# Performance work log

Measured on AMD Instinct MI355X. Metric: run time of the kernel, lower is better.

The kernel has to match this reference:

```python
import jax, jax.numpy as jnp
import numpy as np

# Dimensions
B_, T_, IN_ = 8, 1024, 512          # batch, seq_len, in_dim
D_ = 1024                           # latent_dim (hidden_size)
I_ = 2048                           # intermediate_size
N_ = 64                             # state_size
H_ = 16                             # ssm_num_head
P_ = I_ // H_                       # head_dim = 128
K_ = 3                              # conv_kernel
L_ = 4                              # num_layer
OUT_, CB_ = 512, 1024               # out_dim, num_code_book
CONV_DIM = I_ + 2 * N_              # 2176
PROJ = I_ + CONV_DIM + H_           # in_proj width of mixer = 4240


def setup_inputs() -> dict:
    key = jax.random.key(0)
    ks = jax.random.split(key, 16)
    s = 0.02
    inp = {
        "x": jax.random.normal(ks[0], (B_, T_, IN_), jnp.float32),
        "in_w": jax.random.normal(ks[1], (IN_, D_), jnp.float32) * s,
        "in_b": jnp.zeros((D_,), jnp.float32),
        "norm_w": jnp.ones((L_, D_), jnp.float32),
        "mix_in_w": jax.random.normal(ks[2], (L_, D_, PROJ), jnp.float32) * s,
        "conv_w": jax.random.normal(ks[3], (L_, K_, 1, CONV_DIM), jnp.float32) * s,
        "conv_b": jnp.zeros((L_, CONV_DIM), jnp.float32),
        "dt_bias": jax.random.normal(ks[4], (L_, H_), jnp.float32) * 0.1,
        "A_log": jnp.log(jax.random.uniform(ks[5], (L_, H_), jnp.float32, 0.001, 0.1)),
        "D": jnp.ones((L_, H_), jnp.float32),
        "gnorm_w": jnp.ones((L_, I_), jnp.float32),
        "mix_out_w": jax.random.normal(ks[6], (L_, I_, D_), jnp.float32) * s,
        "out_w": jax.random.normal(ks[7], (D_, OUT_), jnp.float32) * s,
        "out_b": jnp.zeros((OUT_,), jnp.float32),
        "code_w": jax.random.normal(ks[8], (D_, CB_), jnp.float32) * s,
        "code_b": jnp.zeros((CB_,), jnp.float32),
    }
    return inp


def rmsnorm(x, w, eps=1e-6):
    v = jnp.mean(jnp.square(x), axis=-1, keepdims=True)
    return x * jax.lax.rsqrt(v + eps) * w


def mamba_block(x, nw, inw, cw, cb, dtb, alog, Dv, gnw, outw):
    residual = x
    h = rmsnorm(x, nw)
    proj = h @ inw                                   # [B,T,PROJ]
    gate, hBC, dt = jnp.split(proj, [I_, I_ + CONV_DIM], axis=-1)
    # causal depthwise conv along time
    conv = jax.lax.conv_general_dilated(
        hBC, cw, window_strides=(1,), padding=[(K_ - 1, 0)],
        dimension_numbers=("NWC", "WIO", "NWC"), feature_group_count=CONV_DIM)
    conv = jax.nn.silu(conv + cb)
    xs, Bm, Cm = jnp.split(conv, [I_, I_ + N_], axis=-1)   # [B,T,I],[B,T,N],[B,T,N]
    dt = jax.nn.softplus(dt + dtb)                   # [B,T,H]
    a = -jnp.exp(alog)                               # [H] scalar decay per head
    xh = xs.reshape(B_, T_, H_, P_)

    def step(hst, inp):
        dt_t, B_t, C_t, x_t = inp                    # [B,H],[B,N],[B,N],[B,H,P]
        dA = jnp.exp(dt_t * a)                       # [B,H]
        hst = hst * dA[:, :, None, None] + (dt_t[:, :, None, None] * x_t[..., None]) * B_t[:, None, None, :]
        y = jnp.einsum("bhpn,bn->bhp", hst, C_t)
        return hst, y

    inputs = (dt.transpose(1, 0, 2), Bm.transpose(1, 0, 2),
              Cm.transpose(1, 0, 2), xh.transpose(1, 0, 2, 3))
    h0 = jnp.zeros((B_, H_, P_, N_), x.dtype)
    _, ys = jax.lax.scan(step, h0, inputs)           # ys: [T,B,H,P]
    y = ys.transpose(1, 0, 2, 3) + Dv[None, None, :, None] * xh
    y = y.reshape(B_, T_, I_)
    y = rmsnorm(y * jax.nn.silu(gate), gnw)          # gated RMSNorm
    return residual + y @ outw


def reference(x, in_w, in_b, norm_w, mix_in_w, conv_w, conv_b, dt_bias,
              A_log, D, gnorm_w, mix_out_w, out_w, out_b, code_w, code_b):
    h = x @ in_w + in_b
    for i in range(L_):
        h = mamba_block(h, norm_w[i], mix_in_w[i], conv_w[i], conv_b[i],
                        dt_bias[i], A_log[i], D[i], gnorm_w[i], mix_out_w[i])
    return (h @ out_w + out_b, h @ code_w + code_b)
```

## Files before the change

kernel.cpp:

```cpp
#include <hip/hip_runtime.h>
#include <hip/hip_bf16.h>

typedef __hip_bfloat16 bf16;
typedef __bf16 bfv8 __attribute__((ext_vector_type(8)));
typedef float fv4 __attribute__((ext_vector_type(4)));

#define B_  8
#define T_  1024
#define INP 512
#define D_  1024
#define I_  2048
#define N_  64
#define H_  16
#define P_  128
#define L_  4
#define OUT_ 512
#define CB_ 1024
#define CONV_DIM 2176
#define PROJ 4240
#define M_  (B_*T_)
#define TC  64
#define NC  (T_/TC)

typedef const __attribute__((address_space(1))) void gv_t;
typedef __attribute__((address_space(3))) void lv_t;

__device__ __forceinline__ void load_lds16(const bf16* g, char* l) {
    __builtin_amdgcn_global_load_lds((gv_t*)g, (lv_t*)l, 16, 0, 0);
}

template <int N> __device__ __forceinline__ void wait_vm() {
    if constexpr (N == 0)      asm volatile("s_waitcnt vmcnt(0)" ::: "memory");
    else if constexpr (N == 2) asm volatile("s_waitcnt vmcnt(2)" ::: "memory");
    else if constexpr (N == 3) asm volatile("s_waitcnt vmcnt(3)" ::: "memory");
    else if constexpr (N == 4) asm volatile("s_waitcnt vmcnt(4)" ::: "memory");
    else if constexpr (N == 6) asm volatile("s_waitcnt vmcnt(6)" ::: "memory");
    else                       asm volatile("s_waitcnt vmcnt(8)" ::: "memory");
}
__device__ __forceinline__ void barrier_sync() {
    asm volatile("s_barrier" ::: "memory");
}

__device__ __forceinline__ fv4 MF(bfv8 a, bfv8 b, fv4 c) {
    return __builtin_amdgcn_mfma_f32_16x16x32_bf16(a, b, c, 0, 0, 0);
}
__device__ __forceinline__ __bf16 f2b(float x) {
    __hip_bfloat16 h = __float2bfloat16(x);
    union { unsigned short u; __bf16 b; } t;
    t.u = *reinterpret_cast<unsigned short*>(&h);
    return t.b;
}
__device__ __forceinline__ float bb2f(__bf16 x) {
    union { __bf16 b; unsigned short u; } t; t.b = x;
    union { unsigned int u; float f; } r; r.u = (unsigned int)t.u << 16;
    return r.f;
}
__device__ __forceinline__ bfv8 cvt8f(const float* p) {
    float4 a = *(const float4*)p, b = *(const float4*)(p + 4);
    bfv8 r;
    r[0] = f2b(a.x); r[1] = f2b(a.y); r[2] = f2b(a.z); r[3] = f2b(a.w);
    r[4] = f2b(b.x); r[5] = f2b(b.y); r[6] = f2b(b.z); r[7] = f2b(b.w);
    return r;
}

__global__ __launch_bounds__(256) void ingest_k(const float* __restrict__ src,
                                                bf16* __restrict__ dst, int n) {
    int i = blockIdx.x * 256 + threadIdx.x;
    if (i >= n) return;
    dst[i] = __float2bfloat16(src[i]);
}

__global__ __launch_bounds__(256) void transpose_any(const float* __restrict__ in,
                                                     size_t off,
                                                     bf16* __restrict__ out,
                                                     int R, int C) {
    __shared__ bf16 tile[32][33];
    int c0 = blockIdx.x * 32, r0 = blockIdx.y * 32;
    int tx = threadIdx.x, ty = threadIdx.y;
#pragma unroll
    for (int i = 0; i < 4; ++i) {
        int r = r0 + ty + i * 8, c = c0 + tx;
        bf16 v = __float2bfloat16(0.f);
        if (c < C) v = __float2bfloat16(in[off + (size_t)r * C + c]);
        tile[ty + i * 8][tx] = v;
    }
    __syncthreads();
#pragma unroll
    for (int i = 0; i < 4; ++i) {
        int c = c0 + ty + i * 8;
        out[(size_t)c * R + r0 + tx] = tile[tx][ty + i * 8];
    }
}

template <int MODE, int BM, int BN, int WGM, int WGN, int RING, int NTHR>
__global__ __launch_bounds__(NTHR) void gemm8p(const bf16* __restrict__ A,
                                               const bf16* __restrict__ Bt,
                                               int K, int N,
                                               const bf16* __restrict__ bias,
                                               float* __restrict__ outF,
                                               bf16* __restrict__ outB,
                                               bf16* __restrict__ outB2,
                                               float* __restrict__ outF2) {
    constexpr int HK = 32;
    constexpr int MT = BM / WGM / 16;
    constexpr int NT = BN / WGN / 16;
    constexpr int ABY = BM * HK * 2;
    constexpr int BBY = BN * HK * 2;
    constexpr int BUF = ABY + BBY;
    constexpr int RPI = NTHR / 4;
    constexpr int AL = BM / RPI;
    constexpr int BL = BN / RPI;
    constexpr int LD = AL + BL;
    constexpr int IB = NTHR * 16;

    extern __shared__ char lds[];
    const int tid = threadIdx.x;
    const int wv = tid >> 6, lane = tid & 63;
    const int l16 = lane & 15, quad = lane >> 4;
    const int wm = (wv / WGN) * (BM / WGM);
    const int wn = (wv % WGN) * (BN / WGN);

    const int NX = gridDim.x;
    const int nwg = NX * gridDim.y;
    const int orig = blockIdx.y * NX + blockIdx.x;
    const int q = nwg >> 3, r = nwg & 7, xcd = orig & 7, lid = orig >> 3;
    const int wg = (xcd < r ? xcd * (q + 1) : r * (q + 1) + (xcd - r) * q) + lid;
    const int m0 = (wg / NX) * BM;
    const int n0 = (wg % NX) * BN;

    const int srow = tid >> 2, sslot = tid & 3;
    const int swz = (sslot ^ ((srow >> 1) & 3)) << 3;
    const bf16* ga = A  + (size_t)(m0 + srow) * K + swz;
    const bf16* gb = Bt + (size_t)(n0 + srow) * K + swz;
    char* lw = lds + wv * 1024;

    const int HT = K / HK;

    auto stageA = [&](int stg, int rbuf) {
#pragma unroll
        for (int j = 0; j < AL; ++j)
            load_lds16(ga + (size_t)stg * HK + (size_t)(j * RPI) * K,
                       lw + rbuf * BUF + j * IB);
    };
    auto stageB = [&](int stg, int rbuf) {
#pragma unroll
        for (int j = 0; j < BL; ++j)
            load_lds16(gb + (size_t)stg * HK + (size_t)(j * RPI) * K,
                       lw + rbuf * BUF + ABY + j * IB);
    };

#pragma unroll
    for (int h = 0; h < RING - 1; ++h) { stageA(h, h); stageB(h, h); }
    wait_vm<LD>();
    barrier_sync();

    fv4 acc[MT][NT] = {};
    int rb = 0;
    for (int ht = 0; ht < HT; ++ht) {
        const char* Ab = lds + rb * BUF;
        const char* Bb = Ab + ABY;
        const int stg = ht + RING - 1;
        const int sb = (rb == 0) ? RING - 1 : rb - 1;
        const bool dostage = stg < HT;

        bfv8 bf[NT], af[MT];
#pragma unroll
        for (int i = 0; i < NT; ++i) {
            int rr = wn + i * 16 + l16;
            bf[i] = *(const bfv8*)(Bb + rr * 64 + ((quad ^ ((rr >> 1) & 3)) << 4));
        }
#pragma unroll
        for (int i = 0; i < MT; ++i) {
            int rr = wm + i * 16 + l16;
            af[i] = *(const bfv8*)(Ab + rr * 64 + ((quad ^ ((rr >> 1) & 3)) << 4));
        }
        if (dostage) { stageA(stg, sb); stageB(stg, sb); }
        __builtin_amdgcn_s_setprio(1);
#pragma unroll
        for (int mt = 0; mt < MT; ++mt)
#pragma unroll
            for (int nt = 0; nt < NT; ++nt)
                acc[mt][nt] = MF(af[mt], bf[nt], acc[mt][nt]);
        __builtin_amdgcn_s_setprio(0);

        int fut = HT - 1 - ht; if (fut > RING - 1) fut = RING - 1;
        if (fut >= 1) {
            int w = (fut - 1) * LD;
            if (w >= LD) wait_vm<LD>();
            else wait_vm<0>();
        }
        barrier_sync();
        rb = (rb + 1 == RING) ? 0 : rb + 1;
    }

#pragma unroll
    for (int mt = 0; mt < MT; ++mt) {
#pragma unroll
        for (int nt = 0; nt < NT; ++nt) {
#pragma unroll
            for (int i = 0; i < 4; ++i) {
                int row = m0 + wm + mt * 16 + quad * 4 + i;
                int col = n0 + wn + nt * 16 + l16;
                float v = acc[mt][nt][i];
                if (MODE == 0) {
                    v += __bfloat162float(bias[col]);
                    outF[(size_t)row * N + col] = v;
                } else if (MODE == 1) {
                    if (col < I_)
                        outB[(size_t)row * I_ + col] = __float2bfloat16(v);
                    else if (col < I_ + CONV_DIM)
                        outB2[(size_t)row * CONV_DIM + (col - I_)] = __float2bfloat16(v);
                    else if (col < PROJ)
                        outF2[(size_t)row * H_ + (col - (I_ + CONV_DIM))] = v;
                } else if (MODE == 2) {
                    outF[(size_t)row * N + col] += v;
                } else if (MODE == 3) {
                    v += __bfloat162float(bias[col]);
                    if (col < OUT_) outF[(size_t)row * OUT_ + col] = v;
                    else            outF2[(size_t)row * CB_ + (col - OUT_)] = v;
                }
            }
        }
    }
}

__global__ __launch_bounds__(256) void rmsnorm_k(const float* __restrict__ x,
                                                 const bf16* __restrict__ w,
                                                 bf16* __restrict__ out) {
    int row = blockIdx.x, tid = threadIdx.x;
    float4 v = *(const float4*)&x[(size_t)row * D_ + tid * 4];
    float ss = v.x * v.x + v.y * v.y + v.z * v.z + v.w * v.w;
#pragma unroll
    for (int off = 32; off; off >>= 1) ss += __shfl_down(ss, off);
    __shared__ float sb[4];
    if ((tid & 63) == 0) sb[tid >> 6] = ss;
    __syncthreads();
    ss = sb[0] + sb[1] + sb[2] + sb[3];
    float rs = rsqrtf(ss * (1.f / D_) + 1e-6f);
    float xv[4] = {v.x, v.y, v.z, v.w};
#pragma unroll
    for (int j = 0; j < 4; ++j)
        out[(size_t)row * D_ + tid * 4 + j] =
            __float2bfloat16(xv[j] * rs * __bfloat162float(w[tid * 4 + j]));
}

__global__ __launch_bounds__(256) void gatednorm_k(const bf16* __restrict__ y,
                                                   const bf16* __restrict__ g,
                                                   const bf16* __restrict__ w,
                                                   bf16* __restrict__ out) {
    int row = blockIdx.x, tid = threadIdx.x;
    size_t base = (size_t)row * I_ + tid * 8;
    bf16 yv[8], gv[8];
    *(uint4*)yv = *(const uint4*)&y[base];
    *(uint4*)gv = *(const uint4*)&g[base];
    float vv[8]; float ss = 0.f;
#pragma unroll
    for (int j = 0; j < 8; ++j) {
        float yf = __bfloat162float(yv[j]);
        float gf = __bfloat162float(gv[j]);
        float sig = 1.f / (1.f + expf(-gf));
        vv[j] = yf * gf * sig;
        ss += vv[j] * vv[j];
    }
#pragma unroll
    for (int off = 32; off; off >>= 1) ss += __shfl_down(ss, off);
    __shared__ float sb[4];
    if ((tid & 63) == 0) sb[tid >> 6] = ss;
    __syncthreads();
    ss = sb[0] + sb[1] + sb[2] + sb[3];
    float rs = rsqrtf(ss * (1.f / I_) + 1e-6f);
    bf16 ov[8];
#pragma unroll
    for (int j = 0; j < 8; ++j)
        ov[j] = __float2bfloat16(vv[j] * rs * __bfloat162float(w[tid * 8 + j]));
    *(uint4*)&out[base] = *(uint4*)ov;
}

__global__ __launch_bounds__(256) void conv_k(const bf16* __restrict__ hbc,
                                              const bf16* __restrict__ w,
                                              const bf16* __restrict__ bias,
                                              bf16* __restrict__ xs,
                                              float* __restrict__ bc) {
    int cq = blockIdx.x * 32 + (threadIdx.x & 31);
    int btg = blockIdx.y * 8 + (threadIdx.x >> 5);
    int c = cq * 4;
    int bt0 = btg * 8;
    int t0 = bt0 & (T_ - 1);

    bf16 bv[4]; *(uint2*)bv = *(const uint2*)&bias[c];
    float bsf[4];
#pragma unroll
    for (int j = 0; j < 4; ++j) bsf[j] = __bfloat162float(bv[j]);
    float wf[3][4];
#pragma unroll
    for (int k = 0; k < 3; ++k) {
        bf16 wv[4]; *(uint2*)wv = *(const uint2*)&w[k * CONV_DIM + c];
#pragma unroll
        for (int j = 0; j < 4; ++j) wf[k][j] = __bfloat162float(wv[j]);
    }

    float win[10][4];
#pragma unroll
    for (int r = 0; r < 10; ++r) {
        if (t0 - 2 + r < 0) {
#pragma unroll
            for (int j = 0; j < 4; ++j) win[r][j] = 0.f;
        } else {
            bf16 sv[4];
            *(uint2*)sv = *(const uint2*)&hbc[(size_t)(bt0 - 2 + r) * CONV_DIM + c];
#pragma unroll
            for (int j = 0; j < 4; ++j) win[r][j] = __bfloat162float(sv[j]);
        }
    }

#pragma unroll
    for (int i = 0; i < 8; ++i) {
        float acc[4];
#pragma unroll
        for (int j = 0; j < 4; ++j) acc[j] = bsf[j];
#pragma unroll
        for (int k = 0; k < 3; ++k)
#pragma unroll
            for (int j = 0; j < 4; ++j)
                acc[j] = fmaf(wf[k][j], win[i + k][j], acc[j]);
#pragma unroll
        for (int j = 0; j < 4; ++j) acc[j] = acc[j] / (1.f + expf(-acc[j]));
        if (c < I_) {
            bf16 ov[4];
#pragma unroll
            for (int j = 0; j < 4; ++j) ov[j] = __float2bfloat16(acc[j]);
            *(uint2*)&xs[(size_t)(bt0 + i) * I_ + c] = *(uint2*)ov;
        } else {
            float4 o; o.x = acc[0]; o.y = acc[1]; o.z = acc[2]; o.w = acc[3];
            *(float4*)&bc[(size_t)(bt0 + i) * 128 + (c - I_)] = o;
        }
    }
}

__global__ __launch_bounds__(256) void dtprep_k(const float* __restrict__ dtraw,
                                                const float* __restrict__ dtb,
                                                const float* __restrict__ alog,
                                                float* __restrict__ wco,
                                                float* __restrict__ gma) {
    int chain = blockIdx.x * 4 + (threadIdx.x >> 6);
    int s = threadIdx.x & 63;
    int h = chain & 15, ci = (chain >> 4) & (NC - 1), b = chain >> 8;
    float a = -expf(alog[h]);
    float bz = dtb[h];
    int idx = (b * T_ + ci * TC + s) * H_ + h;
    float z = dtraw[idx] + bz;
    float dt = fmaxf(z, 0.f) + log1pf(expf(-fabsf(z)));
    float ps = dt * a;
#pragma unroll
    for (int d = 1; d < 64; d <<= 1) {
        float o = __shfl_up(ps, d, 64);
        if (s >= d) ps += o;
    }
    float g = expf(ps);
    wco[idx] = dt / g;
    gma[idx] = g;
}

__global__ __launch_bounds__(256) void xpose_k(const bf16* __restrict__ in,
                                               bf16* __restrict__ out) {
    __shared__ bf16 tl[64][72];
    int t0 = blockIdx.x * 64;
    int by = blockIdx.y;
    int pg = by & 1, h = (by >> 1) & 15, b = by >> 5;
    int p0 = pg * 64;
    int tx = threadIdx.x & 15, ty = threadIdx.x >> 4;
#pragma unroll
    for (int i = 0; i < 4; ++i) {
        ushort4 v = *(const ushort4*)&in[(size_t)(b * T_ + t0 + ty + 16 * i) * 2048
                                         + h * 128 + p0 + tx * 4];
        tl[ty + 16 * i][tx * 4 + 0] = *(bf16*)&v.x;
        tl[ty + 16 * i][tx * 4 + 1] = *(bf16*)&v.y;
        tl[ty + 16 * i][tx * 4 + 2] = *(bf16*)&v.z;
        tl[ty + 16 * i][tx * 4 + 3] = *(bf16*)&v.w;
    }
    __syncthreads();
#pragma unroll
    for (int i = 0; i < 4; ++i) {
        ushort4 v;
        v.x = *(unsigned short*)&tl[tx * 4 + 0][ty + 16 * i];
        v.y = *(unsigned short*)&tl[tx * 4 + 1][ty + 16 * i];
        v.z = *(unsigned short*)&tl[tx * 4 + 2][ty + 16 * i];
        v.w = *(unsigned short*)&tl[tx * 4 + 3][ty + 16 * i];
        *(ushort4*)&out[(size_t)((b * 16 + h) * 128 + p0 + ty + 16 * i) * 1024
                        + t0 + tx * 4] = v;
    }
}

__global__ __launch_bounds__(256) void btpose_k(const float* __restrict__ in,
                                                bf16* __restrict__ out) {
    __shared__ bf16 tl[64][72];
    int t0 = blockIdx.x * 64;
    int b = blockIdx.y;
    int tx = threadIdx.x & 15, ty = threadIdx.x >> 4;
#pragma unroll
    for (int i = 0; i < 4; ++i) {
        float4 v = *(const float4*)&in[(size_t)(b * T_ + t0 + ty + 16 * i) * 128 + tx * 4];
        tl[ty + 16 * i][tx * 4 + 0] = __float2bfloat16(v.x);
        tl[ty + 16 * i][tx * 4 + 1] = __float2bfloat16(v.y);
        tl[ty + 16 * i][tx * 4 + 2] = __float2bfloat16(v.z);
        tl[ty + 16 * i][tx * 4 + 3] = __float2bfloat16(v.w);
    }
    __syncthreads();
#pragma unroll
    for (int i = 0; i < 4; ++i) {
        ushort4 v;
        v.x = *(unsigned short*)&tl[tx * 4 + 0][ty + 16 * i];
        v.y = *(unsigned short*)&tl[tx * 4 + 1][ty + 16 * i];
        v.z = *(unsigned short*)&tl[tx * 4 + 2][ty + 16 * i];
        v.w = *(unsigned short*)&tl[tx * 4 + 3][ty + 16 * i];
        *(ushort4*)&out[(size_t)(b * 64 + ty + 16 * i) * 1024 + t0 + tx * 4] = v;
    }
}

__global__ __launch_bounds__(256) void scan_mm_k(const float* __restrict__ bc,
                                                 const bf16* __restrict__ xt,
                                                 const bf16* __restrict__ btb,
                                                 const float* __restrict__ wco,
                                                 const float* __restrict__ gma,
                                                 const float* __restrict__ dvec,
                                                 const bf16* __restrict__ xs,
                                                 bf16* __restrict__ yout,
                                                 bf16* __restrict__ sfin) {
    __shared__ __align__(64) char plds[4][8192];
    const int wv = threadIdx.x >> 6, lane = threadIdx.x & 63;
    const int l16 = lane & 15, quad = lane >> 4;
    const int wid = blockIdx.x * 4 + wv;
    const int ci = wid & (NC - 1), h = (wid >> 4) & (H_ - 1), b = wid >> 8;
    const int bt0 = b * T_ + ci * TC;
    char* Pb = plds[wv];

    float wl = wco[(size_t)(bt0 + lane) * H_ + h];
    float gl = gma[(size_t)(bt0 + lane) * H_ + h];
    float g63 = __shfl(gl, 63);
    float Dv = dvec[h];

    float wsv[4], gmv[4][4];
#pragma unroll
    for (int s4 = 0; s4 < 4; ++s4) wsv[s4] = __shfl(wl, s4 * 16 + l16);
#pragma unroll
    for (int t4 = 0; t4 < 4; ++t4)
#pragma unroll
        for (int i = 0; i < 4; ++i) gmv[t4][i] = __shfl(gl, t4 * 16 + quad * 4 + i);

    fv4 g[4][4] = {};
#pragma unroll
    for (int kq = 0; kq < 2; ++kq) {
        bfv8 cf[4], bfr[4];
#pragma unroll
        for (int i = 0; i < 4; ++i) {
            cf[i]  = cvt8f(&bc[(size_t)(bt0 + i * 16 + l16) * 128 + 64 + kq * 32 + quad * 8]);
            bfr[i] = cvt8f(&bc[(size_t)(bt0 + i * 16 + l16) * 128 + kq * 32 + quad * 8]);
        }
#pragma unroll
        for (int t4 = 0; t4 < 4; ++t4)
#pragma unroll
            for (int s4 = 0; s4 < 4; ++s4)
                g[t4][s4] = MF(cf[t4], bfr[s4], g[t4][s4]);
    }

#pragma unroll
    for (int t4 = 0; t4 < 4; ++t4)
#pragma unroll
        for (int s4 = 0; s4 < 4; ++s4)
#pragma unroll
            for (int i = 0; i < 4; ++i) {
                int t = t4 * 16 + quad * 4 + i, s = s4 * 16 + l16;
                float pv = (s <= t) ? g[t4][s4][i] * gmv[t4][i] * wsv[s4] : 0.f;
                int slot = (s >> 3) ^ (t & 7);
                *(__bf16*)(Pb + t * 128 + slot * 16 + (s & 7) * 2) = f2b(pv);
            }

    bfv8 xf[8][2];
    const bf16* xtp = xt + (size_t)((b * 16 + h) * 128) * 1024 + ci * 64;
#pragma unroll
    for (int p4 = 0; p4 < 8; ++p4)
#pragma unroll
        for (int kq = 0; kq < 2; ++kq)
            xf[p4][kq] = *(const bfv8*)&xtp[(size_t)(p4 * 16 + l16) * 1024 + kq * 32 + quad * 8];

    bf16* yp = yout + (size_t)bt0 * I_ + h * P_;
    const bf16* xp = xs + (size_t)bt0 * I_ + h * P_;
#pragma unroll
    for (int t4 = 0; t4 < 4; ++t4) {
        fv4 y[8] = {};
#pragma unroll
        for (int kq = 0; kq < ((t4 < 2) ? 1 : 2); ++kq) {
            int rr = t4 * 16 + l16;
            bfv8 pf = *(const bfv8*)(Pb + rr * 128 + (((kq * 4 + quad) ^ (rr & 7)) << 4));
#pragma unroll
            for (int p4 = 0; p4 < 8; ++p4)
                y[p4] = MF(pf, xf[p4][kq], y[p4]);
        }
#pragma unroll
        for (int p4 = 0; p4 < 8; ++p4)
#pragma unroll
            for (int i = 0; i < 4; ++i) {
                size_t a = (size_t)(t4 * 16 + quad * 4 + i) * I_ + p4 * 16 + l16;
                float xv = __bfloat162float(xp[a]);
                yp[a] = __float2bfloat16(y[p4][i] + Dv * xv);
            }
    }

    float ws8[2][8];
#pragma unroll
    for (int kq = 0; kq < 2; ++kq)
#pragma unroll
        for (int j = 0; j < 8; ++j)
            ws8[kq][j] = g63 * __shfl(wl, kq * 32 + quad * 8 + j);

    fv4 sa[8][4] = {};
    const bf16* btp = btb + (size_t)b * 64 * 1024 + ci * 64;
#pragma unroll
    for (int kq = 0; kq < 2; ++kq) {
        bfv8 sbv[4];
#pragma unroll
        for (int n4 = 0; n4 < 4; ++n4) {
            bfv8 raw = *(const bfv8*)&btp[(size_t)(n4 * 16 + l16) * 1024 + kq * 32 + quad * 8];
            bfv8 sb;
#pragma unroll
            for (int j = 0; j < 8; ++j) sb[j] = f2b(bb2f(raw[j]) * ws8[kq][j]);
            sbv[n4] = sb;
        }
#pragma unroll
        for (int p4 = 0; p4 < 8; ++p4)
#pragma unroll
            for (int n4 = 0; n4 < 4; ++n4)
                sa[p4][n4] = MF(xf[p4][kq], sbv[n4], sa[p4][n4]);
    }

    bf16* sp = sfin + (size_t)wid * (128 * 64);
#pragma unroll
    for (int p4 = 0; p4 < 8; ++p4)
#pragma unroll
        for (int n4 = 0; n4 < 4; ++n4)
#pragma unroll
            for (int i = 0; i < 4; ++i)
                sp[(p4 * 16 + quad * 4 + i) * 64 + n4 * 16 + l16] =
                    __float2bfloat16(sa[p4][n4][i]);
}

__global__ __launch_bounds__(128) void scan_combine_k(bf16* __restrict__ sbuf,
                                                      const float* __restrict__ gma) {
    int bid = blockIdx.x;
    int n = bid & 63;
    int h = (bid >> 6) & (H_ - 1);
    int b = bid >> 10;
    int p = threadIdx.x;
    size_t base0 = ((size_t)(b * (H_ * NC) + h * NC) * (128 * 64)) + n * 128 + p;
    int gbase = b * T_ * H_ + h;
    float S = 0.f;
#pragma unroll
    for (int ci = 0; ci < NC; ++ci) {
        bf16* addr = sbuf + base0 + (size_t)ci * (128 * 64);
        float tmp = __bfloat162float(*addr);
        *addr = __float2bfloat16(S);
        float G = gma[gbase + (ci * TC + TC - 1) * H_];
        S = fmaf(G, S, tmp);
    }
}

__global__ __launch_bounds__(256) void scan_corr_k(const float* __restrict__ bc,
                                                   const bf16* __restrict__ sfin,
                                                   const float* __restrict__ gma,
                                                   bf16* __restrict__ yout) {
    const int wv = threadIdx.x >> 6, lane = threadIdx.x & 63;
    const int wid = blockIdx.x * 4 + wv;
    const int ci = wid & (NC - 1), h = (wid >> 4) & (H_ - 1), b = wid >> 8;
    if (ci == 0) return;
    const int l16 = lane & 15, quad = lane >> 4;
    const int bt0 = b * T_ + ci * TC;

    float gl = gma[(size_t)(bt0 + lane) * H_ + h];
    float gmv[4][4];
#pragma unroll
    for (int t4 = 0; t4 < 4; ++t4)
#pragma unroll
        for (int i = 0; i < 4; ++i) gmv[t4][i] = __shfl(gl, t4 * 16 + quad * 4 + i);

    const bf16* sp = sfin + (size_t)wid * (128 * 64);
    fv4 z[4][8] = {};
#pragma unroll
    for (int kq = 0; kq < 2; ++kq) {
        bfv8 cf[4];
#pragma unroll
        for (int i = 0; i < 4; ++i)
            cf[i] = cvt8f(&bc[(size_t)(bt0 + i * 16 + l16) * 128 + 64 + kq * 32 + quad * 8]);
#pragma unroll
        for (int p4 = 0; p4 < 8; ++p4) {
            bfv8 sf = *(const bfv8*)&sp[(p4 * 16 + l16) * 64 + kq * 32 + quad * 8];
#pragma unroll
            for (int t4 = 0; t4 < 4; ++t4)
                z[t4][p4] = MF(cf[t4], sf, z[t4][p4]);
        }
    }

    bf16* yp = yout + (size_t)bt0 * I_ + h * P_;
#pragma unroll
    for (int t4 = 0; t4 < 4; ++t4)
#pragma unroll
        for (int i = 0; i < 4; ++i) {
            float gm = gmv[t4][i];
#pragma unroll
            for (int p4 = 0; p4 < 8; ++p4) {
                size_t a = (size_t)(t4 * 16 + quad * 4 + i) * I_ + p4 * 16 + l16;
                float yv = __bfloat162float(yp[a]);
                yp[a] = __float2bfloat16(yv + gm * z[t4][p4][i]);
            }
        }
}

__global__ __launch_bounds__(256) void cast_f2b_k(const float* __restrict__ in,
                                                  bf16* __restrict__ out) {
    int i = (blockIdx.x * 256 + threadIdx.x) * 4;
    float4 v = *(const float4*)&in[i];
    bf16 ov[4] = {__float2bfloat16(v.x), __float2bfloat16(v.y),
                  __float2bfloat16(v.z), __float2bfloat16(v.w)};
    *(uint2*)&out[i] = *(uint2*)ov;
}


static inline size_t align256(size_t x) { return (x + 255) & ~(size_t)255; }

extern "C" void kernel_launch(void* const* d_in, const int* in_sizes, int n_in,
                              void* d_out, int out_size, void* d_ws, size_t ws_size,
                              hipStream_t stream) {
    const float* x_in     = (const float*)d_in[0];
    const float* in_w     = (const float*)d_in[1];
    const float* in_b     = (const float*)d_in[2];
    const float* norm_w   = (const float*)d_in[3];
    const float* mix_in_w = (const float*)d_in[4];
    const float* conv_w   = (const float*)d_in[5];
    const float* conv_b   = (const float*)d_in[6];
    const float* dt_bias  = (const float*)d_in[7];
    const float* A_log    = (const float*)d_in[8];
    const float* Dvec     = (const float*)d_in[9];
    const float* gnorm_w  = (const float*)d_in[10];
    const float* mix_out_w= (const float*)d_in[11];
    const float* out_w    = (const float*)d_in[12];
    const float* out_b    = (const float*)d_in[13];
    const float* code_w   = (const float*)d_in[14];
    const float* code_b   = (const float*)d_in[15];
    float* outF0 = (float*)d_out;
    float* outF1 = (float*)d_out + (size_t)M_ * OUT_;

    char* p = (char*)d_ws;
    auto alloc = [&](size_t bytes) -> char* { char* r = p; p += align256(bytes); return r; };

    bf16*  xt       = (bf16*)alloc((size_t)B_ * H_ * 128 * T_ * 2);
    bf16*  hn       = xt;
    bf16*  xb       = xt + (size_t)M_ * D_;
    bf16*  v_inb    = (bf16*)alloc(D_ * 2);
    bf16*  v_normw  = (bf16*)alloc(L_ * D_ * 2);
    bf16*  v_convw  = (bf16*)alloc(L_ * 3 * CONV_DIM * 2);
    bf16*  v_convb  = (bf16*)alloc(L_ * CONV_DIM * 2);
    bf16*  v_gnw    = (bf16*)alloc(L_ * I_ * 2);
    bf16*  v_headb  = (bf16*)alloc((OUT_ + CB_) * 2);
    bf16*  wt_in    = (bf16*)alloc((size_t)1024 * 512 * 2);
    bf16*  wt_big   = (bf16*)alloc((size_t)4352 * 1024 * 2);
    bf16*  wt_small = (bf16*)alloc((size_t)1024 * 2048 * 2);
    bf16*  wt_head  = (bf16*)alloc((size_t)1536 * 1024 * 2);
    float* hbuf     = (float*)alloc((size_t)M_ * D_ * 4);
    bf16*  gate     = (bf16*)alloc((size_t)M_ * I_ * 2);
    bf16*  hbc      = (bf16*)alloc((size_t)M_ * CONV_DIM * 2);
    float* dtraw    = (float*)alloc((size_t)M_ * H_ * 4);
    bf16*  xs       = (bf16*)alloc((size_t)M_ * I_ * 2);
    float* bcbuf    = (float*)alloc((size_t)M_ * 128 * 4);
    float* wcob     = (float*)alloc((size_t)M_ * H_ * 4);
    float* gmab     = (float*)alloc((size_t)M_ * H_ * 4);
    bf16*  sfin     = (bf16*)alloc((size_t)B_ * H_ * NC * 128 * 64 * 2);
    bf16*  bt16     = (bf16*)alloc((size_t)B_ * 64 * T_ * 2);
    (void)in_sizes; (void)n_in; (void)out_size;

    size_t needed = (size_t)(p - (char*)d_ws);
    if (needed > ws_size) return;

    constexpr size_t SH_PROJ = 73728;
    constexpr size_t SH_SQ   = 49152;
    static bool attr_done = false;
    if (!attr_done) {
        attr_done = true;
        (void)hipFuncSetAttribute((const void*)gemm8p<1, 256, 128, 4, 2, 3, 512>,
                                  hipFuncAttributeMaxDynamicSharedMemorySize, (int)SH_PROJ);
        (void)hipFuncSetAttribute((const void*)gemm8p<0, 128, 128, 2, 2, 3, 256>,
                                  hipFuncAttributeMaxDynamicSharedMemorySize, (int)SH_SQ);
        (void)hipFuncSetAttribute((const void*)gemm8p<2, 128, 128, 2, 2, 3, 256>,
                                  hipFuncAttributeMaxDynamicSharedMemorySize, (int)SH_SQ);
        (void)hipFuncSetAttribute((const void*)gemm8p<3, 128, 128, 2, 2, 3, 256>,
                                  hipFuncAttributeMaxDynamicSharedMemorySize, (int)SH_SQ);
    }

    auto ing = [&](const float* src, bf16* dst, int n) {
        ingest_k<<<(n + 255) / 256, 256, 0, stream>>>(src, dst, n);
    };
    ing(x_in, xb, M_ * INP);
    ing(in_b, v_inb, D_);
    ing(norm_w, v_normw, L_ * D_);
    ing(conv_w, v_convw, L_ * 3 * CONV_DIM);
    ing(conv_b, v_convb, L_ * CONV_DIM);
    ing(gnorm_w, v_gnw, L_ * I_);
    ing(out_b, v_headb, OUT_);
    ing(code_b, v_headb + OUT_, CB_);

    dim3 tb(32, 8);
    transpose_any<<<dim3(32, 16), tb, 0, stream>>>(in_w, 0, wt_in, 512, 1024);
    transpose_any<<<dim3(16, 32), tb, 0, stream>>>(out_w, 0, wt_head, 1024, 512);
    transpose_any<<<dim3(32, 32), tb, 0, stream>>>(code_w, 0, wt_head + (size_t)512 * 1024,
                                                   1024, 1024);

    gemm8p<0, 128, 128, 2, 2, 3, 256><<<dim3(8, 64), 256, SH_SQ, stream>>>(
        xb, wt_in, INP, D_, v_inb, hbuf, nullptr, nullptr, nullptr);

    for (int i = 0; i < L_; ++i) {
        transpose_any<<<dim3(136, 32), tb, 0, stream>>>(mix_in_w, (size_t)i * 1024 * PROJ,
                                                        wt_big, 1024, PROJ);
        transpose_any<<<dim3(32, 64), tb, 0, stream>>>(mix_out_w, (size_t)i * 2048 * 1024,
                                                       wt_small, 2048, 1024);
        rmsnorm_k<<<M_, 256, 0, stream>>>(hbuf, v_normw + i * D_, hn);
        gemm8p<1, 256, 128, 4, 2, 3, 512><<<dim3(34, 32), 512, SH_PROJ, stream>>>(
            hn, wt_big, D_, 4352, nullptr, nullptr, gate, hbc, dtraw);
        conv_k<<<dim3(17, 128), 256, 0, stream>>>(hbc, v_convw + i * 3 * CONV_DIM,
                                                  v_convb + i * CONV_DIM, xs, bcbuf);
        dtprep_k<<<B_ * NC * H_ / 4, 256, 0, stream>>>(
            dtraw, dt_bias + i * H_, A_log + i * H_, wcob, gmab);
        xpose_k<<<dim3(16, 256), 256, 0, stream>>>(xs, xt);
        btpose_k<<<dim3(16, 8), 256, 0, stream>>>(bcbuf, bt16);
        scan_mm_k<<<512, 256, 0, stream>>>(bcbuf, xt, bt16, wcob, gmab,
                                           Dvec + i * H_, xs, hbc, sfin);
        scan_combine_k<<<B_ * H_ * 64, 128, 0, stream>>>(sfin, gmab);
        scan_corr_k<<<512, 256, 0, stream>>>(bcbuf, sfin, gmab, hbc);
        gatednorm_k<<<M_, 256, 0, stream>>>(hbc, gate, v_gnw + i * I_, xs);
        gemm8p<2, 128, 128, 2, 2, 3, 256><<<dim3(8, 64), 256, SH_SQ, stream>>>(
            xs, wt_small, I_, D_, nullptr, hbuf, nullptr, nullptr, nullptr);
    }

    cast_f2b_k<<<(M_ * D_) / 1024, 256, 0, stream>>>(hbuf, hn);
    gemm8p<3, 128, 128, 2, 2, 3, 256><<<dim3(12, 64), 256, SH_SQ, stream>>>(
        hn, wt_head, D_, 1536, v_headb, outF0, nullptr, nullptr, outF1);
}
```

Before: 1.587 ms.

## Fuse x and B transposes into conv kernel; shrink in-proj GEMM warp config

The causal conv kernel now also writes the time-major transposed x (xt) and the bf16 transposed B matrix (bt16) directly from its registers, since each thread already holds 8 consecutive timesteps per channel. This removes the separate xpose_k and btpose_k launches and their extra global read of xs/bcbuf. The writes are 16-byte per channel and strided by 1024 elements, so they are less coalesced than the shared-memory transpose was. Separately, the in-projection GEMM changes from 4x2 warps with 512 threads to 2x2 warps with 256 threads on the same 256x128 tile, which doubles per-warp work and register pressure.

Result: slower. 1.639 ms (+3.3%).

```diff
diff --git a/kernel.cpp b/kernel.cpp
--- a/kernel.cpp
+++ b/kernel.cpp
@@ -280,12 +280,15 @@
                                               const bf16* __restrict__ w,
                                               const bf16* __restrict__ bias,
                                               bf16* __restrict__ xs,
-                                              float* __restrict__ bc) {
+                                              float* __restrict__ bc,
+                                              bf16* __restrict__ xt,
+                                              bf16* __restrict__ bt16) {
     int cq = blockIdx.x * 32 + (threadIdx.x & 31);
     int btg = blockIdx.y * 8 + (threadIdx.x >> 5);
     int c = cq * 4;
     int bt0 = btg * 8;
     int t0 = bt0 & (T_ - 1);
+    int b = bt0 >> 10;
 
     bf16 bv[4]; *(uint2*)bv = *(const uint2*)&bias[c];
     float bsf[4];
@@ -313,26 +316,51 @@
         }
     }
 
+    float o[8][4];
 #pragma unroll
     for (int i = 0; i < 8; ++i) {
-        float acc[4];
-#pragma unroll
-        for (int j = 0; j < 4; ++j) acc[j] = bsf[j];
+#pragma unroll
+        for (int j = 0; j < 4; ++j) o[i][j] = bsf[j];
 #pragma unroll
         for (int k = 0; k < 3; ++k)
 #pragma unroll
             for (int j = 0; j < 4; ++j)
-                acc[j] = fmaf(wf[k][j], win[i + k][j], acc[j]);
-#pragma unroll
-        for (int j = 0; j < 4; ++j) acc[j] = acc[j] / (1.f + expf(-acc[j]));
-        if (c < I_) {
+                o[i][j] = fmaf(wf[k][j], win[i + k][j], o[i][j]);
+#pragma unroll
+        for (int j = 0; j < 4; ++j) o[i][j] = o[i][j] / (1.f + expf(-o[i][j]));
+    }
+
+    if (c < I_) {
+#pragma unroll
+        for (int i = 0; i < 8; ++i) {
             bf16 ov[4];
 #pragma unroll
-            for (int j = 0; j < 4; ++j) ov[j] = __float2bfloat16(acc[j]);
+            for (int j = 0; j < 4; ++j) ov[j] = __float2bfloat16(o[i][j]);
             *(uint2*)&xs[(size_t)(bt0 + i) * I_ + c] = *(uint2*)ov;
-        } else {
-            float4 o; o.x = acc[0]; o.y = acc[1]; o.z = acc[2]; o.w = acc[3];
-            *(float4*)&bc[(size_t)(bt0 + i) * 128 + (c - I_)] = o;
+        }
+#pragma unroll
+        for (int j = 0; j < 4; ++j) {
+            int cc = c + j, h = cc >> 7, p = cc & 127;
+            bf16 tv[8];
+#pragma unroll
+            for (int i = 0; i < 8; ++i) tv[i] = __float2bfloat16(o[i][j]);
+            *(uint4*)&xt[(size_t)((b * 16 + h) * 128 + p) * 1024 + t0] = *(uint4*)tv;
+        }
+    } else {
+#pragma unroll
+        for (int i = 0; i < 8; ++i) {
+            float4 fo; fo.x = o[i][0]; fo.y = o[i][1]; fo.z = o[i][2]; fo.w = o[i][3];
+            *(float4*)&bc[(size_t)(bt0 + i) * 128 + (c - I_)] = fo;
+        }
+        if (c < I_ + 64) {
+#pragma unroll
+            for (int j = 0; j < 4; ++j) {
+                int n = c + j - I_;
+                bf16 tv[8];
+#pragma unroll
+                for (int i = 0; i < 8; ++i) tv[i] = __float2bfloat16(o[i][j]);
+                *(uint4*)&bt16[(size_t)(b * 64 + n) * 1024 + t0] = *(uint4*)tv;
+            }
         }
     }
 }
@@ -359,62 +387,6 @@
     float g = expf(ps);
     wco[idx] = dt / g;
     gma[idx] = g;
-}
-
-__global__ __launch_bounds__(256) void xpose_k(const bf16* __restrict__ in,
-                                               bf16* __restrict__ out) {
-    __shared__ bf16 tl[64][72];
-    int t0 = blockIdx.x * 64;
-    int by = blockIdx.y;
-    int pg = by & 1, h = (by >> 1) & 15, b = by >> 5;
-    int p0 = pg * 64;
-    int tx = threadIdx.x & 15, ty = threadIdx.x >> 4;
-#pragma unroll
-    for (int i = 0; i < 4; ++i) {
-        ushort4 v = *(const ushort4*)&in[(size_t)(b * T_ + t0 + ty + 16 * i) * 2048
-                                         + h * 128 + p0 + tx * 4];
-        tl[ty + 16 * i][tx * 4 + 0] = *(bf16*)&v.x;
-        tl[ty + 16 * i][tx * 4 + 1] = *(bf16*)&v.y;
-        tl[ty + 16 * i][tx * 4 + 2] = *(bf16*)&v.z;
-        tl[ty + 16 * i][tx * 4 + 3] = *(bf16*)&v.w;
-    }
-    __syncthreads();
-#pragma unroll
-    for (int i = 0; i < 4; ++i) {
-        ushort4 v;
-        v.x = *(unsigned short*)&tl[tx * 4 + 0][ty + 16 * i];
-        v.y = *(unsigned short*)&tl[tx * 4 + 1][ty + 16 * i];
-        v.z = *(unsigned short*)&tl[tx * 4 + 2][ty + 16 * i];
-        v.w = *(unsigned short*)&tl[tx * 4 + 3][ty + 16 * i];
-        *(ushort4*)&out[(size_t)((b * 16 + h) * 128 + p0 + ty + 16 * i) * 1024
-                        + t0 + tx * 4] = v;
-    }
-}
-
-__global__ __launch_bounds__(256) void btpose_k(const float* __restrict__ in,
-                                                bf16* __restrict__ out) {
-    __shared__ bf16 tl[64][72];
-    int t0 = blockIdx.x * 64;
-    int b = blockIdx.y;
-    int tx = threadIdx.x & 15, ty = threadIdx.x >> 4;
-#pragma unroll
-    for (int i = 0; i < 4; ++i) {
-        float4 v = *(const float4*)&in[(size_t)(b * T_ + t0 + ty + 16 * i) * 128 + tx * 4];
-        tl[ty + 16 * i][tx * 4 + 0] = __float2bfloat16(v.x);
-        tl[ty + 16 * i][tx * 4 + 1] = __float2bfloat16(v.y);
-        tl[ty + 16 * i][tx * 4 + 2] = __float2bfloat16(v.z);
-        tl[ty + 16 * i][tx * 4 + 3] = __float2bfloat16(v.w);
-    }
-    __syncthreads();
-#pragma unroll
-    for (int i = 0; i < 4; ++i) {
-        ushort4 v;
-        v.x = *(unsigned short*)&tl[tx * 4 + 0][ty + 16 * i];
-        v.y = *(unsigned short*)&tl[tx * 4 + 1][ty + 16 * i];
-        v.z = *(unsigned short*)&tl[tx * 4 + 2][ty + 16 * i];
-        v.w = *(unsigned short*)&tl[tx * 4 + 3][ty + 16 * i];
-        *(ushort4*)&out[(size_t)(b * 64 + ty + 16 * i) * 1024 + t0 + tx * 4] = v;
-    }
 }
 
 __global__ __launch_bounds__(256) void scan_mm_k(const float* __restrict__ bc,
@@ -684,7 +656,7 @@
     static bool attr_done = false;
     if (!attr_done) {
         attr_done = true;
-        (void)hipFuncSetAttribute((const void*)gemm8p<1, 256, 128, 4, 2, 3, 512>,
+        (void)hipFuncSetAttribute((const void*)gemm8p<1, 256, 128, 2, 2, 3, 256>,
                                   hipFuncAttributeMaxDynamicSharedMemorySize, (int)SH_PROJ);
         (void)hipFuncSetAttribute((const void*)gemm8p<0, 128, 128, 2, 2, 3, 256>,
                                   hipFuncAttributeMaxDynamicSharedMemorySize, (int)SH_SQ);
@@ -721,14 +693,13 @@
         transpose_any<<<dim3(32, 64), tb, 0, stream>>>(mix_out_w, (size_t)i * 2048 * 1024,
                                                        wt_small, 2048, 1024);
         rmsnorm_k<<<M_, 256, 0, stream>>>(hbuf, v_normw + i * D_, hn);
-        gemm8p<1, 256, 128, 4, 2, 3, 512><<<dim3(34, 32), 512, SH_PROJ, stream>>>(
+        gemm8p<1, 256, 128, 2, 2, 3, 256><<<dim3(34, 32), 256, SH_PROJ, stream>>>(
             hn, wt_big, D_, 4352, nullptr, nullptr, gate, hbc, dtraw);
         conv_k<<<dim3(17, 128), 256, 0, stream>>>(hbc, v_convw + i * 3 * CONV_DIM,
-                                                  v_convb + i * CONV_DIM, xs, bcbuf);
+                                                  v_convb + i * CONV_DIM, xs, bcbuf,
+                                                  xt, bt16);
         dtprep_k<<<B_ * NC * H_ / 4, 256, 0, stream>>>(
             dtraw, dt_bias + i * H_, A_log + i * H_, wcob, gmab);
-        xpose_k<<<dim3(16, 256), 256, 0, stream>>>(xs, xt);
-        btpose_k<<<dim3(16, 8), 256, 0, stream>>>(bcbuf, bt16);
         scan_mm_k<<<512, 256, 0, stream>>>(bcbuf, xt, bt16, wcob, gmab,
                                            Dvec + i * H_, xs, hbc, sfin);
         scan_combine_k<<<B_ * H_ * 64, 128, 0, stream>>>(sfin, gmab);
```
